# Optimization experiments

Measured on AMD Instinct MI355X. Metric: run time of the kernel, lower is better.

The kernel has to match this reference:

```python
import jax, jax.numpy as jnp
import numpy as np
import math

NUM_HEADS = 16


def setup_inputs() -> dict:
    key = jax.random.key(0)
    ks = jax.random.split(key, 5)
    L, B, E = 2048, 2, 1024
    scale = 1.0 / math.sqrt(E)
    return {
        "query": jax.random.normal(ks[0], (L, B, E), jnp.float32),
        "key": jax.random.normal(ks[1], (L, B, E), jnp.float32),
        "value": jax.random.normal(ks[2], (L, B, E), jnp.float32),
        "in_proj_weight": jax.random.normal(ks[3], (3 * E, E), jnp.float32) * scale,
        "in_proj_bias": jnp.zeros((3 * E,), jnp.float32),
        "out_w": jax.random.normal(ks[4], (E, E), jnp.float32) * scale,
        "out_b": jnp.zeros((E,), jnp.float32),
    }


def reference(query, key, value, in_proj_weight, in_proj_bias, out_w, out_b):
    L, Bz, E = query.shape
    S = key.shape[0]
    H = NUM_HEADS
    hd = E // H
    # in-projection: chunk packed weight into q/k/v parts (same math as torch chunk)
    w_q, w_k, w_v = jnp.split(in_proj_weight, 3, axis=0)
    b_q, b_k, b_v = jnp.split(in_proj_bias, 3, axis=0)
    q = query @ w_q.T + b_q            # (L, B, E)
    k = key @ w_k.T + b_k              # (S, B, E)
    v = value @ w_v.T + b_v            # (S, B, E)
    # (L, B*H, hd) -> (B*H, L, hd)
    q = q.reshape(L, Bz * H, hd).transpose(1, 0, 2) / math.sqrt(hd)
    k = k.reshape(S, Bz * H, hd).transpose(1, 0, 2)
    v = v.reshape(S, Bz * H, hd).transpose(1, 0, 2)
    # sigmoid attention (non-softmax), full (B*H, L, S) matrix as in original
    attn = jax.nn.sigmoid(jnp.einsum("bld,bsd->bls", q, k))
    denom = attn.sum(axis=-1, keepdims=True) + 1e-4
    out = jnp.einsum("bls,bsd->bld", attn / denom, v)  # (B*H, L, hd)
    out = out.transpose(1, 0, 2).reshape(L, Bz, E)
    out = out @ out_w.T + out_b
    avg_weights = attn.reshape(Bz, H, L, S).sum(axis=1) / H
    return out, avg_weights
```

## Files before the change

### kernel.cpp

```cpp
#include <hip/hip_runtime.h>
#include <stdint.h>


#define L_SEQ 2048
#define NBATCH 2
#define EMB 1024
#define NHEAD 16
#define HD 64
#define MROWS 4096

typedef __bf16 bf16x8 __attribute__((ext_vector_type(8)));
typedef float f32x4 __attribute__((ext_vector_type(4)));

#define WAITVM(N) asm volatile("s_waitcnt vmcnt(" #N ")" ::: "memory")
#define WAITLG() asm volatile("s_waitcnt lgkmcnt(0)" ::: "memory")
#define SBAR()                                  \
  do {                                          \
    asm volatile("" ::: "memory");              \
    __builtin_amdgcn_s_barrier();               \
    asm volatile("" ::: "memory");              \
  } while (0)

__device__ __forceinline__ unsigned short f2bf(float f) {
  union { float f; uint32_t u; } v; v.f = f;
  uint32_t u = v.u;
  u += 0x7fffu + ((u >> 16) & 1u);
  return (unsigned short)(u >> 16);
}

__device__ __forceinline__ unsigned short f2bf_fast(float f) {
  union { float f; uint32_t u; } v; v.f = f;
  return (unsigned short)((v.u + 0x8000u) >> 16);
}

__device__ __forceinline__ void gl_lds16(const void* gptr, void* ldsptr) {
  const uint32_t* g = reinterpret_cast<const uint32_t*>(gptr);
  auto* l = reinterpret_cast<__attribute__((address_space(3))) uint32_t*>(
      reinterpret_cast<uintptr_t>(ldsptr));
  __builtin_amdgcn_global_load_lds(g, l, 16, 0, 0);
}

__device__ __forceinline__ f32x4 mfma16(bf16x8 a, bf16x8 b, f32x4 c) {
  return __builtin_amdgcn_mfma_f32_16x16x32_bf16(a, b, c, 0, 0, 0);
}

__device__ __forceinline__ float fast_sigmoid(float x) {
  float e = __expf(-x);
  return __builtin_amdgcn_rcpf(1.0f + e);
}

__global__ __launch_bounds__(256) void k_convert(
    const float* __restrict__ qin, const float* __restrict__ kin,
    const float* __restrict__ vin, const float* __restrict__ win,
    const float* __restrict__ wo,
    unsigned short* __restrict__ Xq, unsigned short* __restrict__ Xk,
    unsigned short* __restrict__ Xv, unsigned short* __restrict__ Wb,
    unsigned short* __restrict__ Wob) {
  const int row = blockIdx.x;
  const int t = threadIdx.x;
  const float* src;
  unsigned short* dst;
  int srow;
  size_t drow;
  if (row < 3 * MROWS) {
    const int which = row >> 12;
    const int m = row & (MROWS - 1);
    const int b = m >> 11, l = m & (L_SEQ - 1);
    srow = l * NBATCH + b;
    drow = (size_t)m;
    src = which == 0 ? qin : (which == 1 ? kin : vin);
    dst = which == 0 ? Xq : (which == 1 ? Xk : Xv);
  } else if (row < 3 * MROWS + 3072) {
    srow = row - 3 * MROWS; drow = (size_t)srow; src = win; dst = Wb;
  } else {
    srow = row - (3 * MROWS + 3072); drow = (size_t)srow; src = wo; dst = Wob;
  }
  const float4 vv = *(const float4*)(src + (size_t)srow * EMB + t * 4);
  ushort4 o;
  o.x = f2bf(vv.x); o.y = f2bf(vv.y); o.z = f2bf(vv.z); o.w = f2bf(vv.w);
  *(ushort4*)(dst + drow * EMB + t * 4) = o;
}

__device__ __forceinline__ void gemm_core(
    const unsigned short* __restrict__ A, const unsigned short* __restrict__ Bm,
    int m0, int n0, unsigned short* sA, unsigned short* sB, f32x4 acc[4][4]) {
  const int tid = threadIdx.x;
  const int wave = tid >> 6;
  const int lane = tid & 63;
  const int quad = lane >> 4;
  const int l16 = lane & 15;
  const int wm = (wave >> 1) * 64;
  const int wn = (wave & 1) * 64;
  const int srow = lane >> 2;
  const int scol = lane & 3;

  for (int mi = 0; mi < 4; ++mi)
    for (int ni = 0; ni < 4; ++ni)
      acc[mi][ni] = (f32x4){0.f, 0.f, 0.f, 0.f};

  for (int k0 = 0; k0 < EMB; k0 += 32) {
    __syncthreads();
    for (int i = 0; i < 2; ++i) {
      const int p = wave * 2 + i;
      const int r = p * 16 + srow;
      const int c = scol ^ ((r >> 1) & 3);
      gl_lds16(A + (size_t)(m0 + r) * EMB + k0 + c * 8, sA + p * 512);
      gl_lds16(Bm + (size_t)(n0 + r) * EMB + k0 + c * 8, sB + p * 512);
    }
    __syncthreads();
    bf16x8 af[4], bfr[4];
    for (int mi = 0; mi < 4; ++mi) {
      const int r = wm + mi * 16 + l16;
      const int cp = quad ^ ((r >> 1) & 3);
      af[mi] = *(const bf16x8*)(sA + r * 32 + cp * 8);
    }
    for (int ni = 0; ni < 4; ++ni) {
      const int r = wn + ni * 16 + l16;
      const int cp = quad ^ ((r >> 1) & 3);
      bfr[ni] = *(const bf16x8*)(sB + r * 32 + cp * 8);
    }
    for (int mi = 0; mi < 4; ++mi)
      for (int ni = 0; ni < 4; ++ni)
        acc[mi][ni] = mfma16(af[mi], bfr[ni], acc[mi][ni]);
  }
}

__global__ __launch_bounds__(256) void k_inproj(
    const unsigned short* __restrict__ Xq, const unsigned short* __restrict__ Xk,
    const unsigned short* __restrict__ Xv, const unsigned short* __restrict__ Wb,
    const float* __restrict__ bias,
    unsigned short* __restrict__ qb, unsigned short* __restrict__ kb,
    unsigned short* __restrict__ vb) {
  __shared__ __attribute__((aligned(16))) unsigned short sA[128 * 32];
  __shared__ __attribute__((aligned(16))) unsigned short sB[128 * 32];
  const int z = blockIdx.z;
  const unsigned short* A = z == 0 ? Xq : (z == 1 ? Xk : Xv);
  const int n0 = blockIdx.x * 128, m0 = blockIdx.y * 128;
  f32x4 acc[4][4];
  gemm_core(A, Wb + (size_t)z * EMB * EMB, m0, n0, sA, sB, acc);

  const int tid = threadIdx.x, wave = tid >> 6, lane = tid & 63;
  const int quad = lane >> 4, l16 = lane & 15;
  const int wm = (wave >> 1) * 64, wn = (wave & 1) * 64;
  const float scale = (z == 0) ? 0.125f : 1.0f;
  unsigned short* dst01 = (z == 0) ? qb : kb;
  for (int ni = 0; ni < 4; ++ni) {
    const int n = n0 + wn + ni * 16 + l16;
    const float bv = bias[z * EMB + n];
    const int h = n >> 6, d = n & 63;
    for (int mi = 0; mi < 4; ++mi) {
      for (int r = 0; r < 4; ++r) {
        const int m = m0 + wm + mi * 16 + quad * 4 + r;
        const int b = m >> 11, l = m & (L_SEQ - 1);
        const unsigned short o = f2bf((acc[mi][ni][r] + bv) * scale);
        if (z == 2)
          vb[((size_t)(b * NHEAD + h) * HD + d) * L_SEQ + l] = o;
        else
          dst01[((size_t)(b * NHEAD + h) * L_SEQ + l) * HD + d] = o;
      }
    }
  }
}

__global__ __launch_bounds__(512) void k_attn(
    const unsigned short* __restrict__ qb, const unsigned short* __restrict__ kb,
    const unsigned short* __restrict__ vb, unsigned short* __restrict__ oh) {
  __shared__ __attribute__((aligned(16))) unsigned short sQ[128 * 64];
  __shared__ __attribute__((aligned(16))) unsigned short sK[2][64 * 64];
  __shared__ __attribute__((aligned(16))) unsigned short sV[2][64 * 64];
  __shared__ __attribute__((aligned(16))) unsigned short sP[128 * 72];

  const int bh = blockIdx.x;
  const int b = bh >> 4, h = bh & 15;
  const int l0 = blockIdx.y * 128;
  const unsigned short* qg = qb + ((size_t)bh * L_SEQ + l0) * HD;
  const unsigned short* kg = kb + (size_t)bh * L_SEQ * HD;
  const unsigned short* vg = vb + (size_t)bh * HD * L_SEQ;

  const int tid = threadIdx.x, wave = tid >> 6, lane = tid & 63;
  const int quad = lane >> 4, l16 = lane & 15;
  const int sr8 = lane >> 3, sc8 = lane & 7;
  const int sh = (wave >> 2) * 32;
  const int lq = (wave & 3) * 32;

  for (int i = 0; i < 2; ++i) {
    const int p = wave * 2 + i;
    const int r = p * 8 + sr8;
    const int c = sc8 ^ (r & 7);
    gl_lds16(qg + (size_t)r * HD + c * 8, sQ + p * 512);
  }
  if (wave < 4) {
    for (int i = 0; i < 2; ++i) {
      const int p = wave * 2 + i;
      const int r = p * 8 + sr8;
      const int c = sc8 ^ (r & 7);
      gl_lds16(kg + (size_t)r * HD + c * 8, sK[0] + p * 512);
    }
  } else {
    for (int i = 0; i < 2; ++i) {
      const int p = (wave - 4) * 2 + i;
      const int r = p * 8 + sr8;
      const int c = sc8 ^ (r & 7);
      gl_lds16(vg + (size_t)r * L_SEQ + c * 8, sV[0] + p * 512);
    }
  }

  f32x4 oacc[4];
  for (int ni = 0; ni < 4; ++ni) oacc[ni] = (f32x4){0.f, 0.f, 0.f, 0.f};
  f32x4 dacc = (f32x4){0.f, 0.f, 0.f, 0.f};

  bf16x8 ones;
  for (int j = 0; j < 8; ++j) ones[j] = (__bf16)1.0f;

  const int NS = L_SEQ / 64;
  for (int it = 0; it < NS; ++it) {
    const int cur = it & 1;
    if (it + 1 < NS) {
      const int s0n = (it + 1) * 64;
      if (wave < 4) {
        for (int i = 0; i < 2; ++i) {
          const int p = wave * 2 + i;
          const int r = p * 8 + sr8;
          const int c = sc8 ^ (r & 7);
          gl_lds16(kg + (size_t)(s0n + r) * HD + c * 8, sK[cur ^ 1] + p * 512);
        }
      } else {
        for (int i = 0; i < 2; ++i) {
          const int p = (wave - 4) * 2 + i;
          const int r = p * 8 + sr8;
          const int c = sc8 ^ (r & 7);
          gl_lds16(vg + (size_t)r * L_SEQ + s0n + c * 8, sV[cur ^ 1] + p * 512);
        }
      }
      WAITVM(2);
    } else {
      WAITVM(0);
    }
    SBAR();

    f32x4 st[2][2];
    for (int smi = 0; smi < 2; ++smi)
      for (int lni = 0; lni < 2; ++lni) st[smi][lni] = (f32x4){0.f, 0.f, 0.f, 0.f};
    for (int kk = 0; kk < HD; kk += 32) {
      bf16x8 a[2], bq[2];
      for (int smi = 0; smi < 2; ++smi) {
        const int r = sh + smi * 16 + l16;
        const int c = ((kk >> 3) + quad) ^ (r & 7);
        a[smi] = *(const bf16x8*)(sK[cur] + r * 64 + c * 8);
      }
      for (int lni = 0; lni < 2; ++lni) {
        const int r = lq + lni * 16 + l16;
        const int c = ((kk >> 3) + quad) ^ (r & 7);
        bq[lni] = *(const bf16x8*)(sQ + r * 64 + c * 8);
      }
      for (int smi = 0; smi < 2; ++smi)
        for (int lni = 0; lni < 2; ++lni)
          st[smi][lni] = mfma16(a[smi], bq[lni], st[smi][lni]);
    }

    for (int lni = 0; lni < 2; ++lni) {
      const int lrow = lq + lni * 16 + l16;
      for (int smi = 0; smi < 2; ++smi) {
        uint32_t u[4];
        for (int r = 0; r < 4; ++r) {
          union { float f; uint32_t i; } cv;
          cv.f = fast_sigmoid(st[smi][lni][r]);
          u[r] = cv.i + 0x8000u;
        }
        uint2 pk;
        pk.x = __builtin_amdgcn_perm(u[1], u[0], 0x07060302u);
        pk.y = __builtin_amdgcn_perm(u[3], u[2], 0x07060302u);
        *(uint2*)(sP + (size_t)lrow * 72 + sh + smi * 16 + quad * 4) = pk;
      }
    }
    WAITLG();
    SBAR();

    const int lr = wave * 16 + l16;
    for (int kk = 0; kk < 64; kk += 32) {
      bf16x8 ap = *(const bf16x8*)(sP + (size_t)lr * 72 + kk + quad * 8);
      for (int ni = 0; ni < 4; ++ni) {
        const int rd = ni * 16 + l16;
        const int c = ((kk >> 3) + quad) ^ (rd & 7);
        bf16x8 bv4 = *(const bf16x8*)(sV[cur] + rd * 64 + c * 8);
        oacc[ni] = mfma16(ap, bv4, oacc[ni]);
      }
      dacc = mfma16(ap, ones, dacc);
    }
    SBAR();
  }

  for (int r = 0; r < 4; ++r) {
    const int lrow = l0 + wave * 16 + quad * 4 + r;
    const float rden = __builtin_amdgcn_rcpf(dacc[r] + 1e-4f);
    unsigned short* dst = oh + ((size_t)(b * L_SEQ + lrow)) * EMB + h * HD;
    for (int ni = 0; ni < 4; ++ni)
      dst[ni * 16 + l16] = f2bf_fast(oacc[ni][r] * rden);
  }
}

__global__ __launch_bounds__(512) void k_avg(
    const unsigned short* __restrict__ qb, const unsigned short* __restrict__ kb,
    float* __restrict__ avg) {
  __shared__ __attribute__((aligned(16))) unsigned short sQ[2][128 * 64];
  __shared__ __attribute__((aligned(16))) unsigned short sK[2][128 * 64];
  const int ss0 = blockIdx.x * 128, l0 = blockIdx.y * 128, b = blockIdx.z;
  const int tid = threadIdx.x, wave = tid >> 6, lane = tid & 63;
  const int quad = lane >> 4, l16 = lane & 15;
  const int wm = (wave & 1) * 64, wn = (wave >> 1) * 32;
  const int sr8 = lane >> 3, sc8 = lane & 7;

  f32x4 av[4][2];
  for (int mi = 0; mi < 4; ++mi)
    for (int ni = 0; ni < 2; ++ni) av[mi][ni] = (f32x4){0.f, 0.f, 0.f, 0.f};

  {
    const unsigned short* qg = qb + ((size_t)(b * NHEAD) * L_SEQ + l0) * HD;
    const unsigned short* kg = kb + ((size_t)(b * NHEAD) * L_SEQ + ss0) * HD;
    for (int i = 0; i < 2; ++i) {
      const int p = wave * 2 + i;
      const int r = p * 8 + sr8;
      const int c = sc8 ^ (r & 7);
      gl_lds16(qg + (size_t)r * HD + c * 8, sQ[0] + p * 512);
      gl_lds16(kg + (size_t)r * HD + c * 8, sK[0] + p * 512);
    }
  }

  for (int h = 0; h < NHEAD; ++h) {
    const int cur = h & 1;
    if (h + 1 < NHEAD) {
      const unsigned short* qg =
          qb + ((size_t)(b * NHEAD + h + 1) * L_SEQ + l0) * HD;
      const unsigned short* kg =
          kb + ((size_t)(b * NHEAD + h + 1) * L_SEQ + ss0) * HD;
      for (int i = 0; i < 2; ++i) {
        const int p = wave * 2 + i;
        const int r = p * 8 + sr8;
        const int c = sc8 ^ (r & 7);
        gl_lds16(qg + (size_t)r * HD + c * 8, sQ[cur ^ 1] + p * 512);
        gl_lds16(kg + (size_t)r * HD + c * 8, sK[cur ^ 1] + p * 512);
      }
      WAITVM(4);
    } else {
      WAITVM(0);
    }
    SBAR();

    f32x4 scr[4][2];
    for (int mi = 0; mi < 4; ++mi)
      for (int ni = 0; ni < 2; ++ni) scr[mi][ni] = (f32x4){0.f, 0.f, 0.f, 0.f};
    for (int kk = 0; kk < HD; kk += 32) {
      bf16x8 a[4], bb[2];
      for (int mi = 0; mi < 4; ++mi) {
        const int r = wm + mi * 16 + l16;
        const int c = ((kk >> 3) + quad) ^ (r & 7);
        a[mi] = *(const bf16x8*)(sQ[cur] + r * 64 + c * 8);
      }
      for (int ni = 0; ni < 2; ++ni) {
        const int r = wn + ni * 16 + l16;
        const int c = ((kk >> 3) + quad) ^ (r & 7);
        bb[ni] = *(const bf16x8*)(sK[cur] + r * 64 + c * 8);
      }
      for (int mi = 0; mi < 4; ++mi)
        for (int ni = 0; ni < 2; ++ni)
          scr[mi][ni] = mfma16(a[mi], bb[ni], scr[mi][ni]);
    }
    for (int mi = 0; mi < 4; ++mi)
      for (int ni = 0; ni < 2; ++ni)
        for (int r = 0; r < 4; ++r)
          av[mi][ni][r] += fast_sigmoid(scr[mi][ni][r]);
    SBAR();
  }

  for (int mi = 0; mi < 4; ++mi) {
    for (int r = 0; r < 4; ++r) {
      const int l = l0 + wm + mi * 16 + quad * 4 + r;
      float* dst = avg + ((size_t)b * L_SEQ + l) * L_SEQ + ss0 + wn;
      for (int ni = 0; ni < 2; ++ni)
        dst[ni * 16 + l16] = av[mi][ni][r] * 0.0625f;
    }
  }
}

__global__ __launch_bounds__(256) void k_outproj(
    const unsigned short* __restrict__ OH, const unsigned short* __restrict__ Wob,
    const float* __restrict__ ob, float* __restrict__ out) {
  __shared__ __attribute__((aligned(16))) unsigned short sA[128 * 32];
  __shared__ __attribute__((aligned(16))) unsigned short sB[128 * 32];
  const int n0 = blockIdx.x * 128, m0 = blockIdx.y * 128;
  f32x4 acc[4][4];
  gemm_core(OH, Wob, m0, n0, sA, sB, acc);

  const int tid = threadIdx.x, wave = tid >> 6, lane = tid & 63;
  const int quad = lane >> 4, l16 = lane & 15;
  const int wm = (wave >> 1) * 64, wn = (wave & 1) * 64;
  for (int ni = 0; ni < 4; ++ni) {
    const int n = n0 + wn + ni * 16 + l16;
    const float bv = ob[n];
    for (int mi = 0; mi < 4; ++mi) {
      for (int r = 0; r < 4; ++r) {
        const int m = m0 + wm + mi * 16 + quad * 4 + r;
        const int b = m >> 11, l = m & (L_SEQ - 1);
        out[((size_t)l * NBATCH + b) * EMB + n] = acc[mi][ni][r] + bv;
      }
    }
  }
}

extern "C" void kernel_launch(void* const* d_in, const int* in_sizes, int n_in,
                              void* d_out, int out_size, void* d_ws, size_t ws_size,
                              hipStream_t stream) {
  (void)in_sizes; (void)n_in; (void)out_size;
  const float* qin = (const float*)d_in[0];
  const float* kin = (const float*)d_in[1];
  const float* vin = (const float*)d_in[2];
  const float* w   = (const float*)d_in[3];
  const float* bias = (const float*)d_in[4];
  const float* wo  = (const float*)d_in[5];
  const float* ob  = (const float*)d_in[6];
  float* out = (float*)d_out;

  unsigned short* Xq  = (unsigned short*)d_ws;
  unsigned short* Xk  = Xq + (size_t)MROWS * EMB;
  unsigned short* Xv  = Xk + (size_t)MROWS * EMB;
  unsigned short* Wb  = Xv + (size_t)MROWS * EMB;
  unsigned short* Wob = Wb + (size_t)3 * EMB * EMB;
  unsigned short* qbuf = Wob + (size_t)EMB * EMB;
  unsigned short* kbuf = qbuf + (size_t)MROWS * EMB;
  unsigned short* vbuf = kbuf + (size_t)MROWS * EMB;
  unsigned short* ohb  = vbuf + (size_t)MROWS * EMB;
  const size_t need = ((size_t)MROWS * EMB * 7 + (size_t)4 * EMB * EMB) * 2;
  if (ws_size < need) return;

  k_convert<<<16384, 256, 0, stream>>>(qin, kin, vin, w, wo, Xq, Xk, Xv, Wb, Wob);
  k_inproj<<<dim3(8, 32, 3), 256, 0, stream>>>(Xq, Xk, Xv, Wb, bias, qbuf, kbuf, vbuf);
  k_attn<<<dim3(32, 16), 512, 0, stream>>>(qbuf, kbuf, vbuf, ohb);
  k_avg<<<dim3(16, 16, 2), 512, 0, stream>>>(qbuf, kbuf, out + (size_t)MROWS * EMB);
  k_outproj<<<dim3(8, 32), 256, 0, stream>>>(ohb, Wob, ob, out);
}
```

Before: 283.5 us.

## Double-buffer GEMM LDS, fold log2e into Q scale, restructure attention waves

The in/out projection GEMMs now double-buffer their LDS tiles, issuing the next k-slice load after a single barrier instead of two barriers per step. The Q scale is changed to -log2(e)/8 so sigmoid can use a raw exp2 builtin with no negate or multiply. The attention kernel gives each wave 16 query rows with all 64 keys, which removes two barriers per iteration around the P buffer. The head-averaging kernel moves its prefetch to after one barrier per head. These changes trade LDS footprint and some load-latency hiding for less synchronisation, and the Q values are now negated and prescaled for every consumer.

```diff
diff --git a/kernel.cpp b/kernel.cpp
--- a/kernel.cpp
+++ b/kernel.cpp
@@ -21,6 +21,12 @@
     asm volatile("" ::: "memory");              \
   } while (0)
 
+#if __has_builtin(__builtin_amdgcn_exp2f)
+#define EXP2F(x) __builtin_amdgcn_exp2f(x)
+#else
+#define EXP2F(x) exp2f(x)
+#endif
+
 __device__ __forceinline__ unsigned short f2bf(float f) {
   union { float f; uint32_t u; } v; v.f = f;
   uint32_t u = v.u;
@@ -44,8 +50,8 @@
   return __builtin_amdgcn_mfma_f32_16x16x32_bf16(a, b, c, 0, 0, 0);
 }
 
-__device__ __forceinline__ float fast_sigmoid(float x) {
-  float e = __expf(-x);
+__device__ __forceinline__ float fast_sigmoid2(float st) {
+  float e = EXP2F(st);
   return __builtin_amdgcn_rcpf(1.0f + e);
 }
 
@@ -81,6 +87,23 @@
   *(ushort4*)(dst + drow * EMB + t * 4) = o;
 }
 
+__device__ __forceinline__ void gemm_issue(
+    const unsigned short* __restrict__ A, const unsigned short* __restrict__ Bm,
+    int m0, int n0, int k0, unsigned short* sA, unsigned short* sB) {
+  const int tid = threadIdx.x;
+  const int wave = tid >> 6;
+  const int lane = tid & 63;
+  const int srow = lane >> 2;
+  const int scol = lane & 3;
+  for (int i = 0; i < 2; ++i) {
+    const int p = wave * 2 + i;
+    const int r = p * 16 + srow;
+    const int c = scol ^ ((r >> 1) & 3);
+    gl_lds16(A + (size_t)(m0 + r) * EMB + k0 + c * 8, sA + p * 512);
+    gl_lds16(Bm + (size_t)(n0 + r) * EMB + k0 + c * 8, sB + p * 512);
+  }
+}
+
 __device__ __forceinline__ void gemm_core(
     const unsigned short* __restrict__ A, const unsigned short* __restrict__ Bm,
     int m0, int n0, unsigned short* sA, unsigned short* sB, f32x4 acc[4][4]) {
@@ -91,33 +114,32 @@
   const int l16 = lane & 15;
   const int wm = (wave >> 1) * 64;
   const int wn = (wave & 1) * 64;
-  const int srow = lane >> 2;
-  const int scol = lane & 3;
 
   for (int mi = 0; mi < 4; ++mi)
     for (int ni = 0; ni < 4; ++ni)
       acc[mi][ni] = (f32x4){0.f, 0.f, 0.f, 0.f};
 
+  gemm_issue(A, Bm, m0, n0, 0, sA, sB);
+
   for (int k0 = 0; k0 < EMB; k0 += 32) {
-    __syncthreads();
-    for (int i = 0; i < 2; ++i) {
-      const int p = wave * 2 + i;
-      const int r = p * 16 + srow;
-      const int c = scol ^ ((r >> 1) & 3);
-      gl_lds16(A + (size_t)(m0 + r) * EMB + k0 + c * 8, sA + p * 512);
-      gl_lds16(Bm + (size_t)(n0 + r) * EMB + k0 + c * 8, sB + p * 512);
-    }
-    __syncthreads();
+    const int cur = (k0 >> 5) & 1;
+    WAITVM(0);
+    SBAR();
+    if (k0 + 32 < EMB)
+      gemm_issue(A, Bm, m0, n0, k0 + 32, sA + (cur ^ 1) * 4096,
+                 sB + (cur ^ 1) * 4096);
+    const unsigned short* cA = sA + cur * 4096;
+    const unsigned short* cB = sB + cur * 4096;
     bf16x8 af[4], bfr[4];
     for (int mi = 0; mi < 4; ++mi) {
       const int r = wm + mi * 16 + l16;
       const int cp = quad ^ ((r >> 1) & 3);
-      af[mi] = *(const bf16x8*)(sA + r * 32 + cp * 8);
+      af[mi] = *(const bf16x8*)(cA + r * 32 + cp * 8);
     }
     for (int ni = 0; ni < 4; ++ni) {
       const int r = wn + ni * 16 + l16;
       const int cp = quad ^ ((r >> 1) & 3);
-      bfr[ni] = *(const bf16x8*)(sB + r * 32 + cp * 8);
+      bfr[ni] = *(const bf16x8*)(cB + r * 32 + cp * 8);
     }
     for (int mi = 0; mi < 4; ++mi)
       for (int ni = 0; ni < 4; ++ni)
@@ -131,8 +153,8 @@
     const float* __restrict__ bias,
     unsigned short* __restrict__ qb, unsigned short* __restrict__ kb,
     unsigned short* __restrict__ vb) {
-  __shared__ __attribute__((aligned(16))) unsigned short sA[128 * 32];
-  __shared__ __attribute__((aligned(16))) unsigned short sB[128 * 32];
+  __shared__ __attribute__((aligned(16))) unsigned short sA[2 * 128 * 32];
+  __shared__ __attribute__((aligned(16))) unsigned short sB[2 * 128 * 32];
   const int z = blockIdx.z;
   const unsigned short* A = z == 0 ? Xq : (z == 1 ? Xk : Xv);
   const int n0 = blockIdx.x * 128, m0 = blockIdx.y * 128;
@@ -142,7 +164,7 @@
   const int tid = threadIdx.x, wave = tid >> 6, lane = tid & 63;
   const int quad = lane >> 4, l16 = lane & 15;
   const int wm = (wave >> 1) * 64, wn = (wave & 1) * 64;
-  const float scale = (z == 0) ? 0.125f : 1.0f;
+  const float scale = (z == 0) ? -0.18033688011112042f : 1.0f;
   unsigned short* dst01 = (z == 0) ? qb : kb;
   for (int ni = 0; ni < 4; ++ni) {
     const int n = n0 + wn + ni * 16 + l16;
@@ -180,8 +202,7 @@
   const int tid = threadIdx.x, wave = tid >> 6, lane = tid & 63;
   const int quad = lane >> 4, l16 = lane & 15;
   const int sr8 = lane >> 3, sc8 = lane & 7;
-  const int sh = (wave >> 2) * 32;
-  const int lq = (wave & 3) * 32;
+  const int W = wave * 16;
 
   for (int i = 0; i < 2; ++i) {
     const int p = wave * 2 + i;
@@ -215,6 +236,8 @@
   const int NS = L_SEQ / 64;
   for (int it = 0; it < NS; ++it) {
     const int cur = it & 1;
+    WAITVM(0);
+    SBAR();
     if (it + 1 < NS) {
       const int s0n = (it + 1) * 64;
       if (wave < 4) {
@@ -232,51 +255,41 @@
           gl_lds16(vg + (size_t)r * L_SEQ + s0n + c * 8, sV[cur ^ 1] + p * 512);
         }
       }
-      WAITVM(2);
-    } else {
-      WAITVM(0);
-    }
-    SBAR();
-
-    f32x4 st[2][2];
-    for (int smi = 0; smi < 2; ++smi)
-      for (int lni = 0; lni < 2; ++lni) st[smi][lni] = (f32x4){0.f, 0.f, 0.f, 0.f};
+    }
+
+    f32x4 st[4];
+    for (int smi = 0; smi < 4; ++smi) st[smi] = (f32x4){0.f, 0.f, 0.f, 0.f};
     for (int kk = 0; kk < HD; kk += 32) {
-      bf16x8 a[2], bq[2];
-      for (int smi = 0; smi < 2; ++smi) {
-        const int r = sh + smi * 16 + l16;
+      bf16x8 a[4], bq;
+      for (int smi = 0; smi < 4; ++smi) {
+        const int r = smi * 16 + l16;
         const int c = ((kk >> 3) + quad) ^ (r & 7);
         a[smi] = *(const bf16x8*)(sK[cur] + r * 64 + c * 8);
       }
-      for (int lni = 0; lni < 2; ++lni) {
-        const int r = lq + lni * 16 + l16;
-        const int c = ((kk >> 3) + quad) ^ (r & 7);
-        bq[lni] = *(const bf16x8*)(sQ + r * 64 + c * 8);
-      }
-      for (int smi = 0; smi < 2; ++smi)
-        for (int lni = 0; lni < 2; ++lni)
-          st[smi][lni] = mfma16(a[smi], bq[lni], st[smi][lni]);
-    }
-
-    for (int lni = 0; lni < 2; ++lni) {
-      const int lrow = lq + lni * 16 + l16;
-      for (int smi = 0; smi < 2; ++smi) {
-        uint32_t u[4];
-        for (int r = 0; r < 4; ++r) {
-          union { float f; uint32_t i; } cv;
-          cv.f = fast_sigmoid(st[smi][lni][r]);
-          u[r] = cv.i + 0x8000u;
-        }
-        uint2 pk;
-        pk.x = __builtin_amdgcn_perm(u[1], u[0], 0x07060302u);
-        pk.y = __builtin_amdgcn_perm(u[3], u[2], 0x07060302u);
-        *(uint2*)(sP + (size_t)lrow * 72 + sh + smi * 16 + quad * 4) = pk;
-      }
+      {
+        const int rq = W + l16;
+        const int cq = ((kk >> 3) + quad) ^ (rq & 7);
+        bq = *(const bf16x8*)(sQ + rq * 64 + cq * 8);
+      }
+      for (int smi = 0; smi < 4; ++smi)
+        st[smi] = mfma16(a[smi], bq, st[smi]);
+    }
+
+    for (int smi = 0; smi < 4; ++smi) {
+      uint32_t u[4];
+      for (int r = 0; r < 4; ++r) {
+        union { float f; uint32_t i; } cv;
+        cv.f = fast_sigmoid2(st[smi][r]);
+        u[r] = cv.i + 0x8000u;
+      }
+      uint2 pk;
+      pk.x = __builtin_amdgcn_perm(u[1], u[0], 0x07060302u);
+      pk.y = __builtin_amdgcn_perm(u[3], u[2], 0x07060302u);
+      *(uint2*)(sP + (size_t)(W + l16) * 72 + smi * 16 + quad * 4) = pk;
     }
     WAITLG();
-    SBAR();
-
-    const int lr = wave * 16 + l16;
+
+    const int lr = W + l16;
     for (int kk = 0; kk < 64; kk += 32) {
       bf16x8 ap = *(const bf16x8*)(sP + (size_t)lr * 72 + kk + quad * 8);
       for (int ni = 0; ni < 4; ++ni) {
@@ -287,7 +300,6 @@
       }
       dacc = mfma16(ap, ones, dacc);
     }
-    SBAR();
   }
 
   for (int r = 0; r < 4; ++r) {
@@ -314,37 +326,25 @@
   for (int mi = 0; mi < 4; ++mi)
     for (int ni = 0; ni < 2; ++ni) av[mi][ni] = (f32x4){0.f, 0.f, 0.f, 0.f};
 
-  {
-    const unsigned short* qg = qb + ((size_t)(b * NHEAD) * L_SEQ + l0) * HD;
-    const unsigned short* kg = kb + ((size_t)(b * NHEAD) * L_SEQ + ss0) * HD;
+  auto stage = [&](int hh, int buf) {
+    const unsigned short* qg = qb + ((size_t)(b * NHEAD + hh) * L_SEQ + l0) * HD;
+    const unsigned short* kg = kb + ((size_t)(b * NHEAD + hh) * L_SEQ + ss0) * HD;
     for (int i = 0; i < 2; ++i) {
       const int p = wave * 2 + i;
       const int r = p * 8 + sr8;
       const int c = sc8 ^ (r & 7);
-      gl_lds16(qg + (size_t)r * HD + c * 8, sQ[0] + p * 512);
-      gl_lds16(kg + (size_t)r * HD + c * 8, sK[0] + p * 512);
-    }
-  }
+      gl_lds16(qg + (size_t)r * HD + c * 8, sQ[buf] + p * 512);
+      gl_lds16(kg + (size_t)r * HD + c * 8, sK[buf] + p * 512);
+    }
+  };
+
+  stage(0, 0);
 
   for (int h = 0; h < NHEAD; ++h) {
     const int cur = h & 1;
-    if (h + 1 < NHEAD) {
-      const unsigned short* qg =
-          qb + ((size_t)(b * NHEAD + h + 1) * L_SEQ + l0) * HD;
-      const unsigned short* kg =
-          kb + ((size_t)(b * NHEAD + h + 1) * L_SEQ + ss0) * HD;
-      for (int i = 0; i < 2; ++i) {
-        const int p = wave * 2 + i;
-        const int r = p * 8 + sr8;
-        const int c = sc8 ^ (r & 7);
-        gl_lds16(qg + (size_t)r * HD + c * 8, sQ[cur ^ 1] + p * 512);
-        gl_lds16(kg + (size_t)r * HD + c * 8, sK[cur ^ 1] + p * 512);
-      }
-      WAITVM(4);
-    } else {
-      WAITVM(0);
-    }
+    WAITVM(0);
     SBAR();
+    if (h + 1 < NHEAD) stage(h + 1, cur ^ 1);
 
     f32x4 scr[4][2];
     for (int mi = 0; mi < 4; ++mi)
@@ -368,8 +368,7 @@
     for (int mi = 0; mi < 4; ++mi)
       for (int ni = 0; ni < 2; ++ni)
         for (int r = 0; r < 4; ++r)
-          av[mi][ni][r] += fast_sigmoid(scr[mi][ni][r]);
-    SBAR();
+          av[mi][ni][r] += fast_sigmoid2(scr[mi][ni][r]);
   }
 
   for (int mi = 0; mi < 4; ++mi) {
@@ -385,8 +384,8 @@
 __global__ __launch_bounds__(256) void k_outproj(
     const unsigned short* __restrict__ OH, const unsigned short* __restrict__ Wob,
     const float* __restrict__ ob, float* __restrict__ out) {
-  __shared__ __attribute__((aligned(16))) unsigned short sA[128 * 32];
-  __shared__ __attribute__((aligned(16))) unsigned short sB[128 * 32];
+  __shared__ __attribute__((aligned(16))) unsigned short sA[2 * 128 * 32];
+  __shared__ __attribute__((aligned(16))) unsigned short sB[2 * 128 * 32];
   const int n0 = blockIdx.x * 128, m0 = blockIdx.y * 128;
   f32x4 acc[4][4];
   gemm_core(OH, Wob, m0, n0, sA, sB, acc);
```

After: 285.1 us. About the same (+0.6%).
